# Performance work log

Hardware: AMD Instinct MI355X
Metric: run time of the kernel (lower is better)

## Reference

```python
import jax, jax.numpy as jnp
import numpy as np

EMBED_DIMS = [8, 16, 8]      # prod = 1024 = embed_dim
HIDDEN_DIMS = [16, 16, 16]   # prod = 4096 = hidden_dim
RANK = 16
B, S = 4, 1024


def _make_cores(key, in_dims, out_dims, rank):
    d = len(in_dims)
    ranks = [1] + [rank] * (d - 1) + [1]
    cores = []
    for k in range(d):
        key, sub = jax.random.split(key)
        shape = (ranks[k], in_dims[k], out_dims[k], ranks[k + 1])
        scale = 1.0 / np.sqrt(in_dims[k] * ranks[k])
        cores.append((scale * jax.random.normal(sub, shape, dtype=jnp.float32)))
    return cores


def setup_inputs() -> dict:
    key = jax.random.key(0)
    k_x, k1, k2, kb1, kb2 = jax.random.split(key, 5)
    x = jax.random.normal(k_x, (B, S, 1024), dtype=jnp.float32)
    fc1 = _make_cores(k1, EMBED_DIMS, HIDDEN_DIMS, RANK)
    fc2 = _make_cores(k2, HIDDEN_DIMS, EMBED_DIMS, RANK)
    b1 = 0.01 * jax.random.normal(kb1, (4096,), dtype=jnp.float32)
    b2 = 0.01 * jax.random.normal(kb2, (1024,), dtype=jnp.float32)
    return {
        "x": x,
        "fc1_c0": fc1[0], "fc1_c1": fc1[1], "fc1_c2": fc1[2], "fc1_b": b1,
        "fc2_c0": fc2[0], "fc2_c1": fc2[1], "fc2_c2": fc2[2], "fc2_b": b2,
    }


def tt_linear(x_flat, cores, bias, in_dims):
    """TT-matrix x batch-of-vectors product. x_flat: [N, prod(in_dims)].

    Cores: core_k has shape [r_{k-1}, n_k, m_k, r_k] with r_0 = r_d = 1.
    Invariant: acc is [r_{k-1}, n_k, rest] with rest laid out as
    (n_{k+1}..n_d, N, m_1..m_{k-1}).
    """
    N = x_flat.shape[0]
    acc = x_flat.reshape((N,) + tuple(in_dims))      # [N, n1..nd]
    acc = jnp.moveaxis(acc, 0, -1)                   # [n1..nd, N]
    acc = acc.reshape(in_dims[0], -1)[None]          # [1, n1, rest]
    d = len(cores)
    for k, c in enumerate(cores):
        # contract previous rank + current input mode
        acc = jnp.einsum('pnR,pnmq->Rmq', acc, c)    # [rest, m_k, r_k]
        if k < d - 1:
            n_next = in_dims[k + 1]
            R, m, q = acc.shape
            acc = acc.reshape(n_next, R // n_next, m, q)
            acc = jnp.transpose(acc, (3, 0, 1, 2)).reshape(q, n_next, -1)
    # final acc: [N * m1..m_{d-1}, m_d, 1] -> [N, M]
    return acc.reshape(N, -1) + bias


def reference(x, fc1_c0, fc1_c1, fc1_c2, fc1_b, fc2_c0, fc2_c1, fc2_c2, fc2_b):
    flat = x.reshape(-1, x.shape[-1])                        # [N, embed_dim]
    z1 = tt_linear(flat, [fc1_c0, fc1_c1, fc1_c2], fc1_b, EMBED_DIMS)   # [N, hidden]
    h1 = jax.nn.gelu(z1, approximate=False)                  # exact erf GELU (torch default)
    z2 = tt_linear(h1, [fc2_c0, fc2_c1, fc2_c2], fc2_b, HIDDEN_DIMS)    # [N, embed]
    return z2.reshape(*x.shape[:-1], z2.shape[-1])
```

## Files before the change

kernel.cpp:

```cpp
#include <hip/hip_runtime.h>
#include <stdint.h>

__device__ __forceinline__ float b2f(unsigned short u) {
    union { uint32_t i; float f; } v; v.i = ((uint32_t)u) << 16; return v.f;
}
__device__ __forceinline__ unsigned short f2b(float f) {
    union { float f; uint32_t i; } v; v.f = f;
    uint32_t r = v.i + 0x7fffu + ((v.i >> 16) & 1u);
    return (unsigned short)(r >> 16);
}

typedef __bf16 bf16x8 __attribute__((ext_vector_type(8)));
typedef float  f32x16 __attribute__((ext_vector_type(16)));

template<int N1, int N2, int N3, int M1, int M2, int M3>
__device__ __forceinline__ void build_W_fused(int blk,
                                              const float* __restrict__ c0,
                                              const float* __restrict__ c1,
                                              const float* __restrict__ c2,
                                              unsigned short* __restrict__ W,
                                              float* __restrict__ S) {
    constexpr int K = N1 * N2 * N3;
    const int n2 = blk / M2;
    const int m2 = blk % M2;

    for (int e = threadIdx.x; e < 16 * N3 * M3; e += 256) {
        const int m3 = e % M3;
        const int n3 = (e / M3) % N3;
        const int r1 = e / (M3 * N3);
        const float* c1p = c1 + ((r1 * N2 + n2) * M2 + m2) * 16;
        float s = 0.f;
#pragma unroll
        for (int r2 = 0; r2 < 16; ++r2)
            s += c1p[r2] * c2[(r2 * N3 + n3) * M3 + m3];
        S[e] = s;
    }
    __syncthreads();

    for (int e = threadIdx.x; e < N1 * M1 * M3; e += 256) {
        const int m3 = e % M3;
        const int m1 = (e / M3) % M1;
        const int n1 = e / (M3 * M1);
        const float* c0p = c0 + (n1 * M1 + m1) * 16;
        float acc[N3] = {};
#pragma unroll
        for (int r1 = 0; r1 < 16; ++r1) {
            const float c0v = c0p[r1];
#pragma unroll
            for (int n3 = 0; n3 < N3; ++n3)
                acc[n3] += c0v * S[(r1 * N3 + n3) * M3 + m3];
        }
        unsigned short ob[N3];
#pragma unroll
        for (int n3 = 0; n3 < N3; ++n3) ob[n3] = f2b(acc[n3]);
        unsigned short* dst = W + (size_t)((m1 * M2 + m2) * M3 + m3) * K
                                + (n1 * N2 + n2) * N3;
#pragma unroll
        for (int c = 0; c < N3 / 8; ++c)
            ((int4*)dst)[c] = ((const int4*)ob)[c];
    }
}

__global__ __launch_bounds__(256)
void prep_all(const float* __restrict__ c10, const float* __restrict__ c11,
              const float* __restrict__ c12,
              const float* __restrict__ c20, const float* __restrict__ c21,
              const float* __restrict__ c22,
              const float* __restrict__ x, unsigned short* __restrict__ xb,
              unsigned short* __restrict__ W1, unsigned short* __restrict__ W2) {
    __shared__ float S[16 * 128];
    const int b = blockIdx.x;
    if (b < 256) {
        build_W_fused<8, 16, 8, 16, 16, 16>(b, c10, c11, c12, W1, S);
    } else if (b < 512) {
        build_W_fused<16, 16, 16, 8, 16, 8>(b - 256, c20, c21, c22, W2, S);
    } else {
        const int t = (b - 512) * 256 + threadIdx.x;
        const float4* p = (const float4*)(x + (size_t)t * 8);
        float4 f0 = p[0], f1 = p[1];
        int4 o;
        o.x = (uint32_t)f2b(f0.x) | ((uint32_t)f2b(f0.y) << 16);
        o.y = (uint32_t)f2b(f0.z) | ((uint32_t)f2b(f0.w) << 16);
        o.z = (uint32_t)f2b(f1.x) | ((uint32_t)f2b(f1.y) << 16);
        o.w = (uint32_t)f2b(f1.z) | ((uint32_t)f2b(f1.w) << 16);
        ((int4*)xb)[t] = o;
    }
}

template<int N3, int M3>
__device__ __forceinline__ void build_T_body(int e,
                                             const float* __restrict__ c1,
                                             const float* __restrict__ c2,
                                             float* __restrict__ T) {
    int m3 = e % M3;
    int t  = e / M3;
    int n3 = t % N3;
    int rm = t / N3;
    float s = 0.f;
#pragma unroll
    for (int r2 = 0; r2 < 16; ++r2)
        s += c1[rm * 16 + r2] * c2[(r2 * N3 + n3) * M3 + m3];
    T[e] = s;
}

__global__ __launch_bounds__(256)
void prep_stage1(const float* __restrict__ c11, const float* __restrict__ c12,
                 float* __restrict__ T1,
                 const float* __restrict__ c21, const float* __restrict__ c22,
                 float* __restrict__ T2,
                 const float* __restrict__ x, unsigned short* __restrict__ xb) {
    const int b = blockIdx.x;
    if (b < 2048) {
        build_T_body<8, 16>(b * 256 + threadIdx.x, c11, c12, T1);
    } else if (b < 4096) {
        build_T_body<16, 8>((b - 2048) * 256 + threadIdx.x, c21, c22, T2);
    } else {
        const int t = (b - 4096) * 256 + threadIdx.x;
        const float4* p = (const float4*)(x + (size_t)t * 8);
        float4 f0 = p[0], f1 = p[1];
        int4 o;
        o.x = (uint32_t)f2b(f0.x) | ((uint32_t)f2b(f0.y) << 16);
        o.y = (uint32_t)f2b(f0.z) | ((uint32_t)f2b(f0.w) << 16);
        o.z = (uint32_t)f2b(f1.x) | ((uint32_t)f2b(f1.y) << 16);
        o.w = (uint32_t)f2b(f1.z) | ((uint32_t)f2b(f1.w) << 16);
        ((int4*)xb)[t] = o;
    }
}

template<int N1, int N2, int N3, int M1, int M2, int M3>
__device__ __forceinline__ void build_W_body(int t,
                                             const float* __restrict__ c0,
                                             const float* __restrict__ T,
                                             unsigned short* __restrict__ W) {
    constexpr int K = N1 * N2 * N3;
    int m3 = t % M3;
    int m2 = (t / M3) % M2;
    int n2 = (t / (M3 * M2)) % N2;
    int m1 = (t / (M3 * M2 * N2)) % M1;
    int n1 =  t / (M3 * M2 * N2 * M1);

    float c0r[16];
    const float4* c0p = (const float4*)(c0 + (n1 * M1 + m1) * 16);
#pragma unroll
    for (int i = 0; i < 4; ++i) ((float4*)c0r)[i] = c0p[i];

    float acc[N3] = {};
#pragma unroll
    for (int r1 = 0; r1 < 16; ++r1) {
        const float* Tp = T + (size_t)(((r1 * 16 + n2) * 16 + m2) * N3) * M3 + m3;
#pragma unroll
        for (int n3 = 0; n3 < N3; ++n3)
            acc[n3] += c0r[r1] * Tp[n3 * M3];
    }

    unsigned short ob[N3];
#pragma unroll
    for (int n3 = 0; n3 < N3; ++n3) ob[n3] = f2b(acc[n3]);

    unsigned short* dst = W + (size_t)((m1 * M2 + m2) * M3 + m3) * K
                            + (n1 * N2 + n2) * N3;
#pragma unroll
    for (int c = 0; c < N3 / 8; ++c)
        ((int4*)dst)[c] = ((const int4*)ob)[c];
}

template<int N1, int N2, int N3, int M1, int M2, int M3>
__global__ __launch_bounds__(256)
void build_W(const float* __restrict__ c0, const float* __restrict__ T,
             unsigned short* __restrict__ W) {
    build_W_body<N1, N2, N3, M1, M2, M3>(blockIdx.x * 256 + threadIdx.x, c0, T, W);
}

template<int BM, int BN, int KCH, int KSTR, int GX, int GY,
         bool DO_GELU, bool ATOMIC>
__global__ __launch_bounds__(256, 4)
void gemm_sb(const unsigned short* __restrict__ A,
             const unsigned short* __restrict__ Bt,
             const float* __restrict__ bias,
             void* __restrict__ Cv,
             int Ncols)
{
    constexpr int BK  = 64;
    constexpr int NT  = KCH / BK;
    constexpr int ASZ = BM * BK;
    constexpr int ACH = BM / 32;
    constexpr int BCH = BN / 32;
    constexpr int FI  = BM / 64, FJ = BN / 64;

    extern __shared__ unsigned short sh[];

    const int tid   = threadIdx.x;
    const int lane  = tid & 63;
    const int wave  = tid >> 6;
    const int m32   = lane & 31;
    const int khalf = lane >> 5;
    const int waveM = (wave >> 1) * (BM / 2);
    const int waveN = (wave & 1) * (BN / 2);
    const int srow  = tid >> 3;
    const int sslot = tid & 7;

    int lin = ((int)blockIdx.z * GY + (int)blockIdx.y) * GX + (int)blockIdx.x;
    const int total = GX * GY * (int)gridDim.z;
    lin = (lin & 7) * (total >> 3) + (lin >> 3);
    const int colBase = (lin % GX) * BN;
    const int rowBase = ((lin / GX) % GY) * BM;
    const int kOff    = (lin / (GX * GY)) * KCH;

#define SB_STAGE(K0_)                                                         \
    {                                                                         \
        _Pragma("unroll")                                                     \
        for (int c = 0; c < ACH; ++c) {                                       \
            const int r  = c * 32 + srow;                                     \
            const int jg = sslot ^ (r & 7) ^ ((r >> 3) & 7);                  \
            const unsigned short* src = A +                                   \
                (size_t)(rowBase + r) * KSTR + (K0_) + jg * 8;                \
            unsigned short* dst = sh + c * 2048 + wave * 512;                 \
            __builtin_amdgcn_global_load_lds(                                 \
                (const __attribute__((address_space(1))) void*)src,           \
                (__attribute__((address_space(3))) void*)dst, 16, 0, 0);      \
        }                                                                     \
        _Pragma("unroll")                                                     \
        for (int c = 0; c < BCH; ++c) {                                       \
            const int r  = c * 32 + srow;                                     \
            const int jg = sslot ^ (r & 7) ^ ((r >> 3) & 7);                  \
            const unsigned short* src = Bt +                                  \
                (size_t)(colBase + r) * KSTR + (K0_) + jg * 8;                \
            unsigned short* dst = sh + ASZ + c * 2048 + wave * 512;           \
            __builtin_amdgcn_global_load_lds(                                 \
                (const __attribute__((address_space(1))) void*)src,           \
                (__attribute__((address_space(3))) void*)dst, 16, 0, 0);      \
        }                                                                     \
    }

    f32x16 acc[FI][FJ] = {};

    for (int t = 0; t < NT; ++t) {
        SB_STAGE(kOff + t * BK)
        __syncthreads();

        const unsigned short* Ab = sh;
        const unsigned short* Bb = sh + ASZ;
#pragma unroll
        for (int ks = 0; ks < 4; ++ks) {
            bf16x8 a_f[FI], b_f[FJ];
            const int g = ks * 2 + khalf;
#pragma unroll
            for (int i = 0; i < FI; ++i) {
                const int r = waveM + i * 32 + m32;
                const int key = (r & 7) ^ ((r >> 3) & 7);
                a_f[i] = *(const bf16x8*)&Ab[r * BK + ((g ^ key) << 3)];
            }
#pragma unroll
            for (int j = 0; j < FJ; ++j) {
                const int r = waveN + j * 32 + m32;
                const int key = (r & 7) ^ ((r >> 3) & 7);
                b_f[j] = *(const bf16x8*)&Bb[r * BK + ((g ^ key) << 3)];
            }
#pragma unroll
            for (int i = 0; i < FI; ++i)
#pragma unroll
                for (int j = 0; j < FJ; ++j)
                    acc[i][j] = __builtin_amdgcn_mfma_f32_32x32x16_bf16(
                        a_f[i], b_f[j], acc[i][j], 0, 0, 0);
        }
        if (t + 1 < NT) __syncthreads();
    }
#undef SB_STAGE

#pragma unroll
    for (int i = 0; i < FI; ++i) {
#pragma unroll
        for (int j = 0; j < FJ; ++j) {
            const int col = colBase + waveN + j * 32 + m32;
            const float bv = ATOMIC ? 0.f : bias[col];
#pragma unroll
            for (int reg = 0; reg < 16; ++reg) {
                const int row = rowBase + waveM + i * 32 +
                                (reg & 3) + 8 * (reg >> 2) + 4 * khalf;
                const size_t off = (size_t)row * Ncols + col;
                if (ATOMIC) {
                    unsafeAtomicAdd((float*)Cv + off, acc[i][j][reg]);
                } else {
                    float z = acc[i][j][reg] + bv;
                    if (DO_GELU)
                        z = 0.5f * z * (1.f + erff(z * 0.70710678118654752f));
                    if (ATOMIC) ((float*)Cv)[off] = z;
                    else if (DO_GELU) ((unsigned short*)Cv)[off] = f2b(z);
                    else ((float*)Cv)[off] = z;
                }
            }
        }
    }
}

#define PC_COMPUTE(BUF)                                                       \
    {                                                                         \
        _Pragma("unroll")                                                     \
        for (int ks = 0; ks < 4; ++ks) {                                      \
            bf16x8 a_f[FI], b_f[FJ];                                          \
            _Pragma("unroll")                                                 \
            for (int i = 0; i < FI; ++i) {                                    \
                const int key = (m32 & 7) ^                                   \
                    (((waveM >> 3) + 4 * i + (m32 >> 3)) & 7);                \
                const int slot = ((ks * 2 + khalf) ^ key) * 8;                \
                a_f[i] = *(const bf16x8*)&As[(BUF) * ASZ +                    \
                          (waveM + i * 32 + m32) * BK + slot];                \
            }                                                                 \
            _Pragma("unroll")                                                 \
            for (int j = 0; j < FJ; ++j) {                                    \
                const int key = (m32 & 7) ^                                   \
                    (((waveN >> 3) + 4 * j + (m32 >> 3)) & 7);                \
                const int slot = ((ks * 2 + khalf) ^ key) * 8;                \
                b_f[j] = *(const bf16x8*)&Bs[(BUF) * BSZ +                    \
                          (waveN + j * 32 + m32) * BK + slot];                \
            }                                                                 \
            _Pragma("unroll")                                                 \
            for (int i = 0; i < FI; ++i)                                      \
                _Pragma("unroll")                                             \
                for (int j = 0; j < FJ; ++j)                                  \
                    acc[i][j] = __builtin_amdgcn_mfma_f32_32x32x16_bf16(      \
                        a_f[i], b_f[j], acc[i][j], 0, 0, 0);                  \
        }                                                                     \
    }

template<int BM, int BN, int KTOT, bool DO_GELU, bool A_F32, bool C_F32>
__global__ __launch_bounds__(512, 4)
void gemm_pc(const void* __restrict__ Av,
             const unsigned short* __restrict__ Bt,
             const float* __restrict__ bias,
             void* __restrict__ Cv,
             int Ncols) {
    constexpr int BK  = 64;
    constexpr int CA  = BM / 8;
    constexpr int CB  = BN / 8;
    constexpr int PA  = CA / 4;
    constexpr int PB  = CB / 4;
    constexpr int FI  = BM / 64;
    constexpr int FJ  = BN / 64;
    constexpr int ASZ = BM * BK;
    constexpr int BSZ = BN * BK;
    __shared__ unsigned short As[2 * ASZ];
    __shared__ unsigned short Bs[2 * BSZ];

    const int tid  = threadIdx.x;
    const int lane = tid & 63;
    const int wave = tid >> 6;
    const int rowBase = blockIdx.y * BM;
    const int colBase = blockIdx.x * BN;

    const int lr    = lane >> 3;
    const int jj    = lane & 7;
    const int m32   = lane & 31;
    const int khalf = lane >> 5;

    if (wave >= 4) {
        const int pw = wave - 4;
#pragma unroll
        for (int it = 0; it < PA; ++it) {
            const int c  = pw * PA + it;
            const int jg = jj ^ lr ^ (c & 7);
            const size_t aoff = (size_t)(rowBase + c * 8 + lr) * KTOT + jg * 8;
            int4 v;
            if (A_F32) {
                const float* ga = (const float*)Av + aoff;
                float4 f0 = *(const float4*)ga;
                float4 f1 = *(const float4*)(ga + 4);
                v.x = (uint32_t)f2b(f0.x) | ((uint32_t)f2b(f0.y) << 16);
                v.y = (uint32_t)f2b(f0.z) | ((uint32_t)f2b(f0.w) << 16);
                v.z = (uint32_t)f2b(f1.x) | ((uint32_t)f2b(f1.y) << 16);
                v.w = (uint32_t)f2b(f1.z) | ((uint32_t)f2b(f1.w) << 16);
            } else {
                v = *(const int4*)((const unsigned short*)Av + aoff);
            }
            *(int4*)&As[c * 512 + lane * 8] = v;
        }
#pragma unroll
        for (int it = 0; it < PB; ++it) {
            const int c  = pw * PB + it;
            const int jg = jj ^ lr ^ (c & 7);
            *(int4*)&Bs[c * 512 + lane * 8] =
                *(const int4*)(Bt + (size_t)(colBase + c * 8 + lr) * KTOT + jg * 8);
        }
        __syncthreads();

        int buf = 1;
        for (int k0 = BK; k0 < KTOT; k0 += BK) {
            int4 aR[PA], bR[PB];
#pragma unroll
            for (int it = 0; it < PA; ++it) {
                const int c  = pw * PA + it;
                const int jg = jj ^ lr ^ (c & 7);
                const size_t aoff = (size_t)(rowBase + c * 8 + lr) * KTOT + k0 + jg * 8;
                if (A_F32) {
                    const float* ga = (const float*)Av + aoff;
                    float4 f0 = *(const float4*)ga;
                    float4 f1 = *(const float4*)(ga + 4);
                    int4 v;
                    v.x = (uint32_t)f2b(f0.x) | ((uint32_t)f2b(f0.y) << 16);
                    v.y = (uint32_t)f2b(f0.z) | ((uint32_t)f2b(f0.w) << 16);
                    v.z = (uint32_t)f2b(f1.x) | ((uint32_t)f2b(f1.y) << 16);
                    v.w = (uint32_t)f2b(f1.z) | ((uint32_t)f2b(f1.w) << 16);
                    aR[it] = v;
                } else {
                    aR[it] = *(const int4*)((const unsigned short*)Av + aoff);
                }
            }
#pragma unroll
            for (int it = 0; it < PB; ++it) {
                const int c  = pw * PB + it;
                const int jg = jj ^ lr ^ (c & 7);
                bR[it] = *(const int4*)(Bt + (size_t)(colBase + c * 8 + lr) * KTOT + k0 + jg * 8);
            }
#pragma unroll
            for (int it = 0; it < PA; ++it) {
                const int c = pw * PA + it;
                *(int4*)&As[buf * ASZ + c * 512 + lane * 8] = aR[it];
            }
#pragma unroll
            for (int it = 0; it < PB; ++it) {
                const int c = pw * PB + it;
                *(int4*)&Bs[buf * BSZ + c * 512 + lane * 8] = bR[it];
            }
            __syncthreads();
            buf ^= 1;
        }
    } else {
        const int waveM = (wave >> 1) * (BM / 2);
        const int waveN = (wave & 1) * (BN / 2);
        f32x16 acc[FI][FJ] = {};

        __syncthreads();

        int cur = 0;
        for (int k0 = BK; k0 < KTOT; k0 += BK) {
            PC_COMPUTE(cur)
            __syncthreads();
            cur ^= 1;
        }
        PC_COMPUTE(cur)

#pragma unroll
        for (int i = 0; i < FI; ++i) {
#pragma unroll
            for (int j = 0; j < FJ; ++j) {
                const int col = colBase + waveN + j * 32 + m32;
                const float bv = bias[col];
#pragma unroll
                for (int reg = 0; reg < 16; ++reg) {
                    const int row = rowBase + waveM + i * 32 +
                                    (reg & 3) + 8 * (reg >> 2) + 4 * khalf;
                    float z = acc[i][j][reg] + bv;
                    if (DO_GELU)
                        z = 0.5f * z * (1.f + erff(z * 0.70710678118654752f));
                    const size_t off = (size_t)row * Ncols + col;
                    if (C_F32) ((float*)Cv)[off] = z;
                    else       ((unsigned short*)Cv)[off] = f2b(z);
                }
            }
        }
    }
}

extern "C" void kernel_launch(void* const* d_in, const int* in_sizes, int n_in,
                              void* d_out, int out_size, void* d_ws, size_t ws_size,
                              hipStream_t stream) {
    const float* x      = (const float*)d_in[0];
    const float* fc1_c0 = (const float*)d_in[1];
    const float* fc1_c1 = (const float*)d_in[2];
    const float* fc1_c2 = (const float*)d_in[3];
    const float* fc1_b  = (const float*)d_in[4];
    const float* fc2_c0 = (const float*)d_in[5];
    const float* fc2_c1 = (const float*)d_in[6];
    const float* fc2_c2 = (const float*)d_in[7];
    const float* fc2_b  = (const float*)d_in[8];

    char* ws = (char*)d_ws;
    const bool big = ws_size >= (48ull << 20);

    constexpr int DLDS = 40 << 10;

    if (big) {
        unsigned short* xb = (unsigned short*)d_out;
        unsigned short* W1 = (unsigned short*)ws;
        unsigned short* W2 = (unsigned short*)(ws + (8u << 20));
        unsigned short* h  = (unsigned short*)(ws + (16u << 20));

        prep_all<<<2560, 256, 0, stream>>>(fc1_c0, fc1_c1, fc1_c2,
                                           fc2_c0, fc2_c1, fc2_c2,
                                           x, xb, W1, W2);
        gemm_sb<128, 128, 1024, 1024, 32, 32, true, false>
            <<<dim3(32, 32, 1), 256, DLDS, stream>>>(xb, W1, fc1_b, h, 4096);
        gemm_sb<128, 64, 4096, 4096, 16, 32, false, false>
            <<<dim3(16, 32, 1), 256, DLDS, stream>>>(h, W2, fc2_b, d_out, 1024);
    } else {
        float* T1 = (float*)d_out;
        float* T2 = (float*)d_out + 524288;
        unsigned short* xb = (unsigned short*)((char*)d_out + (4u << 20));
        unsigned short* W = (unsigned short*)ws;
        unsigned short* h = (unsigned short*)(ws + (8u << 20));

        prep_stage1<<<6144, 256, 0, stream>>>(fc1_c1, fc1_c2, T1,
                                              fc2_c1, fc2_c2, T2, x, xb);
        build_W<8, 16, 8, 16, 16, 16><<<2048, 256, 0, stream>>>(fc1_c0, T1, W);
        gemm_pc<128, 128, 1024, true, false, false>
            <<<dim3(32, 32), 512, 0, stream>>>(xb, W, fc1_b, h, 4096);
        build_W<16, 16, 16, 8, 16, 8><<<1024, 256, 0, stream>>>(fc2_c0, T2, W);
        gemm_pc<128, 64, 4096, false, false, true>
            <<<dim3(16, 32), 512, 0, stream>>>(h, W, fc2_b, d_out, 1024);
    }
}
```

Measured before the change: 211.7 us.

## Add 8-wave triple-buffered GEMM with direct-to-LDS loads for first TT layer

Introduces a new 512-thread GEMM kernel using 256x128 tiles, triple-buffered LDS staging via global_load_lds, interleaved barriers with raised wave priority around MFMA, and a grid swizzle over groups of 8. It replaces the first fused GELU GEMM in the large-workspace path. The aim is better overlap of global loads with matrix math and more reuse per block, at the cost of 144KB LDS per block, lower occupancy and more barriers. The old epilogue branches are also simplified.

```diff
diff --git a/kernel.cpp b/kernel.cpp
--- a/kernel.cpp
+++ b/kernel.cpp
@@ -169,6 +169,130 @@
 void build_W(const float* __restrict__ c0, const float* __restrict__ T,
              unsigned short* __restrict__ W) {
     build_W_body<N1, N2, N3, M1, M2, M3>(blockIdx.x * 256 + threadIdx.x, c0, T, W);
+}
+
+template<int BM, int BN, int KTOT, int GX, bool DO_GELU>
+__global__ __launch_bounds__(512, 2)
+void gemm_8p(const unsigned short* __restrict__ A,
+             const unsigned short* __restrict__ Bt,
+             const float* __restrict__ bias,
+             unsigned short* __restrict__ C,
+             int Ncols)
+{
+    constexpr int BK   = 64;
+    constexpr int NT   = KTOT / BK;
+    constexpr int AE   = BM * BK;
+    constexpr int SLOT = (BM + BN) * BK;
+    constexpr int ACH  = (AE * 2) / 1024;
+    constexpr int CPW  = ((SLOT * 2) / 1024) / 8;
+
+    extern __shared__ unsigned short sh[];
+
+    const int tid   = threadIdx.x;
+    const int lane  = tid & 63;
+    const int wave  = tid >> 6;
+    const int m32   = lane & 31;
+    const int kh    = lane >> 5;
+    const int waveM = (wave >> 1) * 64;
+    const int waveN = (wave & 1) * 64;
+    const int srow8 = lane >> 3;
+    const int sslot = lane & 7;
+
+    int lin = (int)blockIdx.y * GX + (int)blockIdx.x;
+    const int total = GX * (int)gridDim.y;
+    lin = (lin & 7) * (total >> 3) + (lin >> 3);
+    const int colBase = (lin % GX) * BN;
+    const int rowBase = (lin / GX) * BM;
+
+#define P8_STAGE(TS_, KK_, U_)                                                \
+    {                                                                         \
+        const int c_   = wave * CPW + (U_);                                   \
+        const bool b_  = c_ >= ACH;                                           \
+        const int r_   = (b_ ? c_ - ACH : c_) * 8 + srow8;                    \
+        const int jg_  = sslot ^ (r_ & 7) ^ ((r_ >> 3) & 7);                  \
+        const unsigned short* s_ = (b_ ?                                      \
+            Bt + (size_t)(colBase + r_) * KTOT :                              \
+            A  + (size_t)(rowBase + r_) * KTOT) + (KK_) + jg_ * 8;            \
+        unsigned short* d_ = sh + (TS_) + c_ * 512;                           \
+        __builtin_amdgcn_global_load_lds(                                     \
+            (const __attribute__((address_space(1))) void*)s_,                \
+            (__attribute__((address_space(3))) void*)d_, 16, 0, 0);           \
+    }
+
+    f32x16 acc[2][2] = {};
+
+#pragma unroll
+    for (int u = 0; u < CPW; ++u) P8_STAGE(0, 0, u)
+#pragma unroll
+    for (int u = 0; u < CPW; ++u) P8_STAGE(SLOT, BK, u)
+    asm volatile("s_waitcnt vmcnt(%0)" :: "n"(CPW) : "memory");
+    __builtin_amdgcn_s_barrier();
+
+    for (int t = 0; t < NT; ++t) {
+        const unsigned short* Ab = sh + (t % 3) * SLOT;
+        const unsigned short* Bb = Ab + AE;
+        const int ts = ((t + 2) % 3) * SLOT;
+        const int kk = (t + 2) * BK;
+        const bool doStage = (t + 2 < NT);
+
+#pragma unroll
+        for (int ph = 0; ph < 4; ++ph) {
+            bf16x8 af[2], bfr[2];
+            const int g = ph * 2 + kh;
+#pragma unroll
+            for (int i = 0; i < 2; ++i) {
+                const int r = waveM + i * 32 + m32;
+                const int key = (r & 7) ^ ((r >> 3) & 7);
+                af[i] = *(const bf16x8*)&Ab[r * BK + ((g ^ key) << 3)];
+            }
+#pragma unroll
+            for (int j = 0; j < 2; ++j) {
+                const int r = waveN + j * 32 + m32;
+                const int key = (r & 7) ^ ((r >> 3) & 7);
+                bfr[j] = *(const bf16x8*)&Bb[r * BK + ((g ^ key) << 3)];
+            }
+            if (doStage && ph < 3) {
+                P8_STAGE(ts, kk, ph * 2)
+                P8_STAGE(ts, kk, ph * 2 + 1)
+            }
+            __builtin_amdgcn_s_barrier();
+            __builtin_amdgcn_s_setprio(1);
+#pragma unroll
+            for (int i = 0; i < 2; ++i)
+#pragma unroll
+                for (int j = 0; j < 2; ++j)
+                    acc[i][j] = __builtin_amdgcn_mfma_f32_32x32x16_bf16(
+                        af[i], bfr[j], acc[i][j], 0, 0, 0);
+            __builtin_amdgcn_s_setprio(0);
+            __builtin_amdgcn_s_barrier();
+        }
+
+        if (t + 2 < NT) {
+            asm volatile("s_waitcnt vmcnt(%0)" :: "n"(CPW) : "memory");
+        } else if (t + 1 < NT) {
+            asm volatile("s_waitcnt vmcnt(0)" ::: "memory");
+        }
+        if (t + 1 < NT) __builtin_amdgcn_s_barrier();
+    }
+#undef P8_STAGE
+
+#pragma unroll
+    for (int i = 0; i < 2; ++i) {
+#pragma unroll
+        for (int j = 0; j < 2; ++j) {
+            const int col = colBase + waveN + j * 32 + m32;
+            const float bv = bias[col];
+#pragma unroll
+            for (int reg = 0; reg < 16; ++reg) {
+                const int row = rowBase + waveM + i * 32 +
+                                (reg & 3) + 8 * (reg >> 2) + 4 * kh;
+                float z = acc[i][j][reg] + bv;
+                if (DO_GELU)
+                    z = 0.5f * z * (1.f + erff(z * 0.70710678118654752f));
+                C[(size_t)row * Ncols + col] = f2b(z);
+            }
+        }
+    }
 }
 
 template<int BM, int BN, int KCH, int KSTR, int GX, int GY,
@@ -282,11 +406,12 @@
                     unsafeAtomicAdd((float*)Cv + off, acc[i][j][reg]);
                 } else {
                     float z = acc[i][j][reg] + bv;
-                    if (DO_GELU)
+                    if (DO_GELU) {
                         z = 0.5f * z * (1.f + erff(z * 0.70710678118654752f));
-                    if (ATOMIC) ((float*)Cv)[off] = z;
-                    else if (DO_GELU) ((unsigned short*)Cv)[off] = f2b(z);
-                    else ((float*)Cv)[off] = z;
+                        ((unsigned short*)Cv)[off] = f2b(z);
+                    } else {
+                        ((float*)Cv)[off] = z;
+                    }
                 }
             }
         }
@@ -477,7 +602,16 @@
     char* ws = (char*)d_ws;
     const bool big = ws_size >= (48ull << 20);
 
-    constexpr int DLDS = 40 << 10;
+    constexpr int DLDS8 = 3 * (256 + 128) * 64 * 2;
+    constexpr int DLDS  = 40 << 10;
+
+    static bool attr_done = false;
+    if (!attr_done) {
+        attr_done = true;
+        (void)hipFuncSetAttribute(
+            reinterpret_cast<const void*>(&gemm_8p<256, 128, 1024, 32, true>),
+            hipFuncAttributeMaxDynamicSharedMemorySize, DLDS8);
+    }
 
     if (big) {
         unsigned short* xb = (unsigned short*)d_out;
@@ -488,8 +622,8 @@
         prep_all<<<2560, 256, 0, stream>>>(fc1_c0, fc1_c1, fc1_c2,
                                            fc2_c0, fc2_c1, fc2_c2,
                                            x, xb, W1, W2);
-        gemm_sb<128, 128, 1024, 1024, 32, 32, true, false>
-            <<<dim3(32, 32, 1), 256, DLDS, stream>>>(xb, W1, fc1_b, h, 4096);
+        gemm_8p<256, 128, 1024, 32, true>
+            <<<dim3(32, 16), 512, DLDS8, stream>>>(xb, W1, fc1_b, h, 4096);
         gemm_sb<128, 64, 4096, 4096, 16, 32, false, false>
             <<<dim3(16, 32, 1), 256, DLDS, stream>>>(h, W2, fc2_b, d_out, 1024);
     } else {
```

After: 211.0 us. Within noise of the previous version (-0.3%).
